# Optimization experiments

Hardware: AMD Instinct MI355X
Metric: run time of the kernel (lower is better)

Reference implementation:

```python
import jax, jax.numpy as jnp
import numpy as np

RESOLUTION = 0.1
EMPTY = 255.0  # fill value for BEV cells with no point


def setup_inputs() -> dict:
    key = jax.random.key(0)
    k1, k2 = jax.random.split(key)
    B, H, W = 16, 128, 2048
    # labels in [0, 1): float surrogate for the original long labels so the
    # gather->scatter dataflow (the kernel of interest) is identical
    fv_label_img = jax.random.uniform(k1, (B, 1, H, W), dtype=jnp.float32)
    # metric xyz coordinates, ~ +-60 m spread so roughly half land in-grid
    fv_pointcloud = jax.random.normal(k2, (B, 3, H, W), dtype=jnp.float32) * 20.0
    return {
        "fv_label_img": fv_label_img,
        "fv_pointcloud": fv_pointcloud,
        "bev_h": 1024,
        "bev_w": 1024,
        "scale": 1,
    }


def reference(fv_label_img, fv_pointcloud, bev_h, bev_w, scale):
    res = RESOLUTION * scale
    # per-point BEV cell indices (same math as torch: round then cast)
    x_idx = jnp.round(-fv_pointcloud[:, 0] / res + bev_w // 2).astype(jnp.int32)  # [B,H,W]
    z_idx = jnp.round(fv_pointcloud[:, 2] / res).astype(jnp.int32)                # [B,H,W]
    valid = (x_idx >= 0) & (x_idx < bev_w) & (z_idx >= 0) & (z_idx < bev_h)
    # route invalid points out of range so mode='drop' discards them
    z_safe = jnp.where(valid, z_idx, bev_h)
    labels = fv_label_img[:, 0]  # [B,H,W]

    def scatter_one(z, x, lab):
        bev = jnp.full((bev_h, bev_w), EMPTY, dtype=lab.dtype)
        return bev.at[z.reshape(-1), x.reshape(-1)].set(lab.reshape(-1), mode="drop")

    bev = jax.vmap(scatter_one)(z_safe, x_idx, labels)  # [B,bev_h,bev_w]
    return bev[:, None]  # [B,1,bev_h,bev_w]
```

## Files before the change

kernel.cpp:

```cpp
#include <hip/hip_runtime.h>
#include <hip/hip_bf16.h>

__global__ void bev_fill_kernel(float4* __restrict__ out, int n4) {
    int idx = blockIdx.x * blockDim.x + threadIdx.x;
    int stride = gridDim.x * blockDim.x;
    const float4 v = make_float4(255.0f, 255.0f, 255.0f, 255.0f);
    for (int i = idx; i < n4; i += stride) {
        out[i] = v;
    }
}

__global__ void bev_scatter_kernel(const float* __restrict__ labels,
                                   const float* __restrict__ pc,
                                   const int* __restrict__ p_bev_h,
                                   const int* __restrict__ p_bev_w,
                                   const int* __restrict__ p_scale,
                                   float* __restrict__ out,
                                   int n_pts, int out_size) {
    const int bev_h = *p_bev_h;
    const int bev_w = *p_bev_w;
    const int scale = *p_scale;
    const double res_d = 0.1 * (double)scale;
    const float half_w = (float)(bev_w / 2);

    double rd = 1.0 / res_d;
    asm volatile("" : "+v"(rd));

    const int img = bev_h * bev_w;
    const int B = out_size / img;
    const int HW = n_pts / B;

    int t = blockIdx.x * blockDim.x + threadIdx.x;
    int i4 = t * 4;
    if (i4 >= n_pts) return;

    int b = i4 / HW;
    int r = i4 - b * HW;

    const float* pcb = pc + (size_t)b * 3u * (size_t)HW;
    float4 lab = *(const float4*)(labels + i4);
    float4 x0  = *(const float4*)(pcb + r);
    float4 z0  = *(const float4*)(pcb + 2 * (size_t)HW + r);

    float* outb = out + (size_t)b * (size_t)img;

    float xs[4] = {x0.x, x0.y, x0.z, x0.w};
    float zs[4] = {z0.x, z0.y, z0.z, z0.w};
    float ls[4] = {lab.x, lab.y, lab.z, lab.w};

#pragma unroll
    for (int k = 0; k < 4; ++k) {
        float xq = (float)((double)(-xs[k]) * rd);
        float zq = (float)((double)zs[k] * rd);
        float xf = rintf(__fadd_rn(xq, half_w));
        float zf = rintf(zq);
        int xi = (int)xf;
        int zi = (int)zf;
        if (xi >= 0 && xi < bev_w && zi >= 0 && zi < bev_h) {
            outb[(size_t)zi * (size_t)bev_w + (size_t)xi] = ls[k];
        }
    }
}

extern "C" void kernel_launch(void* const* d_in, const int* in_sizes, int n_in,
                              void* d_out, int out_size, void* d_ws, size_t ws_size,
                              hipStream_t stream) {
    const float* labels = (const float*)d_in[0];
    const float* pc     = (const float*)d_in[1];
    const int* p_bev_h  = (const int*)d_in[2];
    const int* p_bev_w  = (const int*)d_in[3];
    const int* p_scale  = (const int*)d_in[4];
    float* out = (float*)d_out;

    int n_pts = in_sizes[0];

    int n4 = out_size / 4;
    bev_fill_kernel<<<2048, 256, 0, stream>>>((float4*)out, n4);

    int n_thr = (n_pts + 3) / 4;
    int blocks = (n_thr + 255) / 256;
    bev_scatter_kernel<<<blocks, 256, 0, stream>>>(labels, pc, p_bev_h, p_bev_w,
                                                   p_scale, out, n_pts, out_size);
}
```

Measured before the change: 45.06 us.

## Map fill and scatter blocks to XCDs by batch for L2 locality

Both the fill and scatter kernels now use a block-to-(batch, chunk) mapping that, when the batch count is a multiple of 8, assigns each batch to one XCD (block index mod 8). Blocks that fill a batch's BEV image and blocks that later scatter into that image then land on the same XCD. This is meant to keep the image lines in that XCD's L2 and cut cross-die traffic and write misses. The fill kernel also switches from a grid-stride loop to one block per 4096 floats, which launches many more blocks, and it relies on the hardware's round-robin dispatch of blocks to XCDs.

```diff
diff --git a/kernel.cpp b/kernel.cpp
--- a/kernel.cpp
+++ b/kernel.cpp
@@ -1,12 +1,40 @@
 #include <hip/hip_runtime.h>
 #include <hip/hip_bf16.h>
 
-__global__ void bev_fill_kernel(float4* __restrict__ out, int n4) {
-    int idx = blockIdx.x * blockDim.x + threadIdx.x;
-    int stride = gridDim.x * blockDim.x;
+__device__ __forceinline__ void map_block(int j, int B, int bpb,
+                                          int& batch, int& chunk) {
+    if ((B & 7) == 0) {
+        int xcd = j & 7;
+        int g = j >> 3;
+        int per = B >> 3;
+        batch = xcd + 8 * (g % per);
+        chunk = g / per;
+    } else {
+        batch = j / bpb;
+        chunk = j - batch * bpb;
+    }
+}
+
+__global__ void bev_fill_kernel(float4* __restrict__ out,
+                                const int* __restrict__ p_bev_h,
+                                const int* __restrict__ p_bev_w,
+                                int out_size) {
+    const int img  = (*p_bev_h) * (*p_bev_w);
+    const int img4 = img >> 2;
+    const int B    = out_size / img;
+    const int bpb  = (img4 + 1023) >> 10;
+
+    int batch, chunk;
+    map_block(blockIdx.x, B, bpb, batch, chunk);
+    if (batch >= B) return;
+
+    float4* dst = out + (size_t)batch * (size_t)img4;
+    int base = (chunk << 10) + threadIdx.x;
     const float4 v = make_float4(255.0f, 255.0f, 255.0f, 255.0f);
-    for (int i = idx; i < n4; i += stride) {
-        out[i] = v;
+#pragma unroll
+    for (int k = 0; k < 4; ++k) {
+        int idx = base + (k << 8);
+        if (idx < img4) dst[idx] = v;
     }
 }
 
@@ -29,20 +57,21 @@
     const int img = bev_h * bev_w;
     const int B = out_size / img;
     const int HW = n_pts / B;
+    const int bpb = (HW + 1023) >> 10;
 
-    int t = blockIdx.x * blockDim.x + threadIdx.x;
-    int i4 = t * 4;
-    if (i4 >= n_pts) return;
+    int batch, chunk;
+    map_block(blockIdx.x, B, bpb, batch, chunk);
+    if (batch >= B) return;
 
-    int b = i4 / HW;
-    int r = i4 - b * HW;
+    int r = ((chunk << 8) + threadIdx.x) << 2;
+    if (r >= HW) return;
 
-    const float* pcb = pc + (size_t)b * 3u * (size_t)HW;
-    float4 lab = *(const float4*)(labels + i4);
+    const float* pcb = pc + (size_t)batch * 3u * (size_t)HW;
+    float4 lab = *(const float4*)(labels + (size_t)batch * (size_t)HW + r);
     float4 x0  = *(const float4*)(pcb + r);
     float4 z0  = *(const float4*)(pcb + 2 * (size_t)HW + r);
 
-    float* outb = out + (size_t)b * (size_t)img;
+    float* outb = out + (size_t)batch * (size_t)img;
 
     float xs[4] = {x0.x, x0.y, x0.z, x0.w};
     float zs[4] = {z0.x, z0.y, z0.z, z0.w};
@@ -74,11 +103,12 @@
 
     int n_pts = in_sizes[0];
 
-    int n4 = out_size / 4;
-    bev_fill_kernel<<<2048, 256, 0, stream>>>((float4*)out, n4);
+    int fill_blocks = (out_size + 4095) / 4096;
+    bev_fill_kernel<<<fill_blocks, 256, 0, stream>>>((float4*)out, p_bev_h,
+                                                     p_bev_w, out_size);
 
-    int n_thr = (n_pts + 3) / 4;
-    int blocks = (n_thr + 255) / 256;
-    bev_scatter_kernel<<<blocks, 256, 0, stream>>>(labels, pc, p_bev_h, p_bev_w,
-                                                   p_scale, out, n_pts, out_size);
+    int sc_blocks = (n_pts + 1023) / 1024;
+    bev_scatter_kernel<<<sc_blocks, 256, 0, stream>>>(labels, pc, p_bev_h,
+                                                      p_bev_w, p_scale, out,
+                                                      n_pts, out_size);
 }
```

Measured after the change: 39.02 us. 13.4% less time.

## Bin points by BEV row band, then assemble output tiles in LDS

Applied to the files above, without the earlier changes.

Replaces the separate fill kernel and random global scatter with two passes. The first pass classifies each 1024-point chunk into 8-row bins using an LDS histogram, a prefix scan and compaction, and writes compact cell/label lists plus offsets to the workspace. The second pass builds each 8-row output tile in LDS, pre-filled with 255, applies the binned points, and writes the tile out coalesced. This removes the full-output fill traffic and the scattered global writes, at the cost of workspace traffic, an extra launch and LDS atomics. Duplicate-cell write order stays nondeterministic, as before.

```diff
diff --git a/kernel.cpp b/kernel.cpp
--- a/kernel.cpp
+++ b/kernel.cpp
@@ -1,63 +1,173 @@
 #include <hip/hip_runtime.h>
 #include <hip/hip_bf16.h>
 
-__global__ void bev_fill_kernel(float4* __restrict__ out, int n4) {
-    int idx = blockIdx.x * blockDim.x + threadIdx.x;
-    int stride = gridDim.x * blockDim.x;
-    const float4 v = make_float4(255.0f, 255.0f, 255.0f, 255.0f);
-    for (int i = idx; i < n4; i += stride) {
-        out[i] = v;
-    }
-}
-
-__global__ void bev_scatter_kernel(const float* __restrict__ labels,
-                                   const float* __restrict__ pc,
-                                   const int* __restrict__ p_bev_h,
-                                   const int* __restrict__ p_bev_w,
-                                   const int* __restrict__ p_scale,
-                                   float* __restrict__ out,
-                                   int n_pts, int out_size) {
-    const int bev_h = *p_bev_h;
-    const int bev_w = *p_bev_w;
-    const int scale = *p_scale;
-    const double res_d = 0.1 * (double)scale;
-    const float half_w = (float)(bev_w / 2);
-
-    double rd = 1.0 / res_d;
-    asm volatile("" : "+v"(rd));
-
+#define BIN_ROWS   8
+#define MAX_BINS   256
+#define OFF_STRIDE 257
+#define P1_PTS     1024
+
+typedef unsigned short u16;
+typedef unsigned int   u32;
+
+__device__ __forceinline__ bool fit_ok(int HW, int bev_h, int bev_w, int ws_ok) {
+    return ws_ok && (HW % P1_PTS == 0) && (bev_h % BIN_ROWS == 0) &&
+           (bev_h / BIN_ROWS <= MAX_BINS) && (bev_w <= 1024) && (bev_w % 4 == 0);
+}
+
+__device__ __forceinline__ void classE(float px, float pz, double rd,
+                                       float half_w, int& xi, int& zi) {
+    float xq = (float)((double)(-px) * rd);
+    float zq = (float)((double)pz  * rd);
+    xi = (int)rintf(__fadd_rn(xq, half_w));
+    zi = (int)rintf(zq);
+}
+
+__global__ __launch_bounds__(256) void kA(const float* __restrict__ labels,
+        const float* __restrict__ pc,
+        const int* __restrict__ p_bev_h, const int* __restrict__ p_bev_w,
+        const int* __restrict__ p_scale, float* __restrict__ out,
+        u16* __restrict__ cell16, float* __restrict__ lab32,
+        u16* __restrict__ offs16, int n_pts, int out_size, int ws_ok) {
+    const int bev_h = *p_bev_h, bev_w = *p_bev_w, scale = *p_scale;
     const int img = bev_h * bev_w;
     const int B = out_size / img;
     const int HW = n_pts / B;
-
-    int t = blockIdx.x * blockDim.x + threadIdx.x;
-    int i4 = t * 4;
-    if (i4 >= n_pts) return;
-
-    int b = i4 / HW;
-    int r = i4 - b * HW;
-
-    const float* pcb = pc + (size_t)b * 3u * (size_t)HW;
-    float4 lab = *(const float4*)(labels + i4);
-    float4 x0  = *(const float4*)(pcb + r);
-    float4 z0  = *(const float4*)(pcb + 2 * (size_t)HW + r);
-
-    float* outb = out + (size_t)b * (size_t)img;
-
-    float xs[4] = {x0.x, x0.y, x0.z, x0.w};
-    float zs[4] = {z0.x, z0.y, z0.z, z0.w};
-    float ls[4] = {lab.x, lab.y, lab.z, lab.w};
-
-#pragma unroll
-    for (int k = 0; k < 4; ++k) {
-        float xq = (float)((double)(-xs[k]) * rd);
-        float zq = (float)((double)zs[k] * rd);
-        float xf = rintf(__fadd_rn(xq, half_w));
-        float zf = rintf(zq);
-        int xi = (int)xf;
-        int zi = (int)zf;
-        if (xi >= 0 && xi < bev_w && zi >= 0 && zi < bev_h) {
-            outb[(size_t)zi * (size_t)bev_w + (size_t)xi] = ls[k];
+    const float half_w = (float)(bev_w / 2);
+    double rd = 1.0 / (0.1 * (double)scale);
+    asm volatile("" : "+v"(rd));
+
+    if (fit_ok(HW, bev_h, bev_w, ws_ok)) {
+        const int nbins = bev_h / BIN_ROWS;
+        const int nblk_pb = HW / P1_PTS;
+        const int nblkTot = B * nblk_pb;
+        int gblk = blockIdx.x;
+        if (gblk >= nblkTot) return;
+        int batch = gblk / nblk_pb;
+        int r = (gblk - batch * nblk_pb) * P1_PTS + threadIdx.x * 4;
+
+        __shared__ u32 hist[MAX_BINS];
+        __shared__ u32 scan[MAX_BINS];
+        __shared__ u16 cellL[P1_PTS];
+        __shared__ float labL[P1_PTS];
+
+        const float* pcb = pc + (size_t)batch * 3u * (size_t)HW;
+        float4 lab = *(const float4*)(labels + (size_t)batch * (size_t)HW + r);
+        float4 x0  = *(const float4*)(pcb + r);
+        float4 z0  = *(const float4*)(pcb + 2 * (size_t)HW + r);
+        float xs[4] = {x0.x, x0.y, x0.z, x0.w};
+        float zs[4] = {z0.x, z0.y, z0.z, z0.w};
+        float ls[4] = {lab.x, lab.y, lab.z, lab.w};
+
+        int bin[4]; u16 cell[4]; bool val[4];
+#pragma unroll
+        for (int k = 0; k < 4; ++k) {
+            int xi, zi; classE(xs[k], zs[k], rd, half_w, xi, zi);
+            val[k]  = (xi >= 0 && xi < bev_w && zi >= 0 && zi < bev_h);
+            bin[k]  = val[k] ? (zi >> 3) : 0;
+            cell[k] = val[k] ? (u16)((zi & 7) * bev_w + xi) : 0;
+        }
+        if ((int)threadIdx.x < nbins) hist[threadIdx.x] = 0;
+        __syncthreads();
+#pragma unroll
+        for (int k = 0; k < 4; ++k) if (val[k]) atomicAdd(&hist[bin[k]], 1u);
+        __syncthreads();
+        u32 v = ((int)threadIdx.x < nbins) ? hist[threadIdx.x] : 0;
+        scan[threadIdx.x] = v;
+        __syncthreads();
+        for (int d = 1; d < MAX_BINS; d <<= 1) {
+            u32 t = (threadIdx.x >= (unsigned)d) ? scan[threadIdx.x - d] : 0;
+            __syncthreads();
+            scan[threadIdx.x] += t;
+            __syncthreads();
+        }
+        if ((int)threadIdx.x < nbins)
+            hist[threadIdx.x] = (threadIdx.x == 0) ? 0 : scan[threadIdx.x - 1];
+        __syncthreads();
+#pragma unroll
+        for (int k = 0; k < 4; ++k) if (val[k]) {
+            u32 pos = atomicAdd(&hist[bin[k]], 1u);
+            cellL[pos] = cell[k];
+            labL[pos]  = ls[k];
+        }
+        __syncthreads();
+        u32 total = scan[nbins - 1];
+        u16* cg = cell16 + (size_t)gblk * P1_PTS;
+        float* lg = lab32 + (size_t)gblk * P1_PTS;
+        for (u32 i = threadIdx.x; i < total; i += 256) {
+            cg[i] = cellL[i];
+            lg[i] = labL[i];
+        }
+        u16* og = offs16 + (size_t)gblk * OFF_STRIDE;
+        for (int j = threadIdx.x; j <= nbins; j += 256)
+            og[j] = (u16)((j == 0) ? 0 : scan[j - 1]);
+    } else {
+        int n4 = out_size >> 2;
+        const float4 vv = make_float4(255.f, 255.f, 255.f, 255.f);
+        for (int i = blockIdx.x * 256 + threadIdx.x; i < n4;
+             i += gridDim.x * 256)
+            ((float4*)out)[i] = vv;
+    }
+}
+
+__global__ __launch_bounds__(256) void kB(const float* __restrict__ labels,
+        const float* __restrict__ pc,
+        const int* __restrict__ p_bev_h, const int* __restrict__ p_bev_w,
+        const int* __restrict__ p_scale, float* __restrict__ out,
+        const u16* __restrict__ cell16, const float* __restrict__ lab32,
+        const u16* __restrict__ offs16, int n_pts, int out_size, int ws_ok) {
+    const int bev_h = *p_bev_h, bev_w = *p_bev_w, scale = *p_scale;
+    const int img = bev_h * bev_w;
+    const int B = out_size / img;
+    const int HW = n_pts / B;
+    const float half_w = (float)(bev_w / 2);
+    double rd = 1.0 / (0.1 * (double)scale);
+    asm volatile("" : "+v"(rd));
+
+    if (fit_ok(HW, bev_h, bev_w, ws_ok)) {
+        const int nbins = bev_h / BIN_ROWS;
+        const int nblk_pb = HW / P1_PTS;
+        const int ntiles = B * nbins;
+        const int nel = BIN_ROWS * bev_w;
+        __shared__ float tile[BIN_ROWS * 1024];
+        for (int t = blockIdx.x; t < ntiles; t += gridDim.x) {
+            int bt = t / nbins, j = t - bt * nbins;
+            for (int i = threadIdx.x; i < nel; i += 256) tile[i] = 255.0f;
+            __syncthreads();
+            for (int s = threadIdx.x; s < nblk_pb; s += 256) {
+                int gblk = bt * nblk_pb + s;
+                const u16* og = offs16 + (size_t)gblk * OFF_STRIDE;
+                int o0 = og[j], o1 = og[j + 1];
+                const u16* cg = cell16 + (size_t)gblk * P1_PTS;
+                const float* lg = lab32 + (size_t)gblk * P1_PTS;
+                for (int i = o0; i < o1; ++i) tile[cg[i]] = lg[i];
+            }
+            __syncthreads();
+            float4* dst = (float4*)(out + (size_t)bt * img + (size_t)j * nel);
+            const float4* src = (const float4*)tile;
+            for (int i = threadIdx.x; i < (nel >> 2); i += 256) dst[i] = src[i];
+            __syncthreads();
+        }
+    } else {
+        int nq = n_pts >> 2;
+        for (int q = blockIdx.x * 256 + threadIdx.x; q < nq;
+             q += gridDim.x * 256) {
+            int i4 = q * 4;
+            int b = i4 / HW;
+            int r = i4 - b * HW;
+            const float* pcb = pc + (size_t)b * 3u * (size_t)HW;
+            float4 lab = *(const float4*)(labels + (size_t)b * (size_t)HW + r);
+            float4 x0  = *(const float4*)(pcb + r);
+            float4 z0  = *(const float4*)(pcb + 2 * (size_t)HW + r);
+            float* outb = out + (size_t)b * (size_t)img;
+            float xs[4] = {x0.x, x0.y, x0.z, x0.w};
+            float zs[4] = {z0.x, z0.y, z0.z, z0.w};
+            float ls[4] = {lab.x, lab.y, lab.z, lab.w};
+#pragma unroll
+            for (int k = 0; k < 4; ++k) {
+                int xi, zi; classE(xs[k], zs[k], rd, half_w, xi, zi);
+                if (xi >= 0 && xi < bev_w && zi >= 0 && zi < bev_h)
+                    outb[(size_t)zi * (size_t)bev_w + (size_t)xi] = ls[k];
+            }
         }
     }
 }
@@ -71,14 +181,25 @@
     const int* p_bev_w  = (const int*)d_in[3];
     const int* p_scale  = (const int*)d_in[4];
     float* out = (float*)d_out;
-
     int n_pts = in_sizes[0];
 
-    int n4 = out_size / 4;
-    bev_fill_kernel<<<2048, 256, 0, stream>>>((float4*)out, n4);
-
-    int n_thr = (n_pts + 3) / 4;
-    int blocks = (n_thr + 255) / 256;
-    bev_scatter_kernel<<<blocks, 256, 0, stream>>>(labels, pc, p_bev_h, p_bev_w,
-                                                   p_scale, out, n_pts, out_size);
-}
+    int nblkTot = (n_pts + P1_PTS - 1) / P1_PTS;
+    size_t cell_bytes = (size_t)nblkTot * P1_PTS * 2;
+    size_t lab_bytes  = (size_t)nblkTot * P1_PTS * 4;
+    size_t off_bytes  = (size_t)nblkTot * OFF_STRIDE * 2;
+    size_t need = cell_bytes + lab_bytes + off_bytes;
+    int ws_ok = (ws_size >= need) ? 1 : 0;
+
+    u16*  cell16 = (u16*)d_ws;
+    float* lab32 = (float*)((char*)d_ws + cell_bytes);
+    u16*  offs16 = (u16*)((char*)d_ws + cell_bytes + lab_bytes);
+
+    int ka_blocks = nblkTot > 2048 ? nblkTot : 2048;
+    kA<<<ka_blocks, 256, 0, stream>>>(labels, pc, p_bev_h, p_bev_w, p_scale,
+                                      out, cell16, lab32, offs16,
+                                      n_pts, out_size, ws_ok);
+
+    kB<<<2048, 256, 0, stream>>>(labels, pc, p_bev_h, p_bev_w, p_scale,
+                                 out, cell16, lab32, offs16,
+                                 n_pts, out_size, ws_ok);
+}
```

Result: slower. 53.93 us (+19.7%).
